# Kernel tuning notes

Measured on AMD Instinct MI355X. Metric: run time of the kernel, lower is better.

## Reference

```python
import jax, jax.numpy as jnp
import numpy as np

POOL_SIZE = 4
MAX_DIM = 256
GRID = MAX_DIM // POOL_SIZE  # 64
NUM_CELLS = GRID * GRID      # 4096
B = 64                        # static max_batch (batch.max()+1 in torch)
N = 1_000_000
C = 64


def setup_inputs() -> dict:
    key = jax.random.key(0)
    k1, k2, k3 = jax.random.split(key, 3)
    x = jax.random.normal(k1, (N, C), dtype=jnp.float32)
    pos = jax.random.randint(k2, (N, 2), 0, MAX_DIM, dtype=jnp.int64)
    batch = jnp.sort(jax.random.randint(k3, (N,), 0, B, dtype=jnp.int64))
    return {"x": x, "pos": pos, "batch": batch}


def reference(x, pos, batch):
    # voxel key: (batch, pos_x//pool, pos_y//pool) -> flat cell index
    qpos = pos[:, :2] // POOL_SIZE                       # [N, 2] int
    idx = batch * NUM_CELLS + qpos[:, 0] * GRID + qpos[:, 1]  # [N]
    num_seg = B * NUM_CELLS
    # scatter_reduce(amax, include_self=False): max over points in each cell
    pooled = jax.ops.segment_max(x, idx, num_segments=num_seg)  # empty -> -inf
    # cells with no points stay zero (output_x initialized to zeros in torch)
    counts = jax.ops.segment_sum(jnp.ones((x.shape[0], 1), x.dtype), idx,
                                 num_segments=num_seg)          # [num_seg, 1]
    pooled = jnp.where(counts > 0, pooled, jnp.zeros((), x.dtype))
    # [B, grid^2, C] -> flatten -> [B, grid^2 * C]
    return pooled.reshape(B, NUM_CELLS * x.shape[1])
```

## Files before the change

kernel.cpp:

```cpp
#include <hip/hip_runtime.h>

#define POOL_SHIFT 2
#define GRID_DIM 64
#define NUM_CELLS 4096
#define NCH 64
#define BATCH 64
#define NSEG (BATCH * NUM_CELLS)
#define SCAN_BLOCKS 1024
#define RANK_BITS 14
#define RANK_MASK ((1u << RANK_BITS) - 1u)

typedef float vf4 __attribute__((ext_vector_type(4)));

__global__ __launch_bounds__(256) void count_kernel(
    const int* __restrict__ pos, const int* __restrict__ batch,
    unsigned int* __restrict__ counts, unsigned int* __restrict__ cellrank, int n) {
    int stride = gridDim.x * blockDim.x;
    for (int p = blockIdx.x * blockDim.x + threadIdx.x; p < n; p += stride) {
        long long t = __builtin_nontemporal_load((const long long*)pos + p);
        int px = (int)t;
        int py = (int)(t >> 32);
        int b  = __builtin_nontemporal_load(&batch[p]);
        int c  = b * NUM_CELLS + (px >> POOL_SHIFT) * GRID_DIM + (py >> POOL_SHIFT);
        unsigned int r = atomicAdd(&counts[c], 1u);
        __builtin_nontemporal_store(((unsigned int)c << RANK_BITS) | r, &cellrank[p]);
    }
}

__global__ __launch_bounds__(256) void reduce_kernel(
    const unsigned int* __restrict__ counts, unsigned int* __restrict__ blocksum) {
    __shared__ unsigned int ws[4];
    int t = threadIdx.x;
    unsigned int v = counts[blockIdx.x * 256 + t];
    #pragma unroll
    for (int off = 1; off < 64; off <<= 1) v += __shfl_xor((int)v, off, 64);
    if ((t & 63) == 0) ws[t >> 6] = v;
    __syncthreads();
    if (t == 0) blocksum[blockIdx.x] = ws[0] + ws[1] + ws[2] + ws[3];
}

__global__ __launch_bounds__(1024) void scanblock_kernel(
    const unsigned int* __restrict__ blocksum, unsigned int* __restrict__ blockbase) {
    __shared__ unsigned int wsum[16];
    int t = threadIdx.x, lane = t & 63, w = t >> 6;
    unsigned int own = blocksum[t];
    unsigned int v = own;
    #pragma unroll
    for (int off = 1; off < 64; off <<= 1) {
        unsigned int u = __shfl_up((int)v, off, 64);
        if (lane >= off) v += u;
    }
    if (lane == 63) wsum[w] = v;
    __syncthreads();
    unsigned int base = 0;
    for (int i = 0; i < w; ++i) base += wsum[i];
    blockbase[t] = v + base - own;
}

__global__ __launch_bounds__(256) void offsets_kernel(
    const unsigned int* __restrict__ counts, const unsigned int* __restrict__ blockbase,
    unsigned int* __restrict__ offsets, int n) {
    __shared__ unsigned int wsum[4];
    int t = threadIdx.x, b = blockIdx.x, lane = t & 63, w = t >> 6;
    unsigned int own = counts[b * 256 + t];
    unsigned int v = own;
    #pragma unroll
    for (int off = 1; off < 64; off <<= 1) {
        unsigned int u = __shfl_up((int)v, off, 64);
        if (lane >= off) v += u;
    }
    if (lane == 63) wsum[w] = v;
    __syncthreads();
    unsigned int base = blockbase[b];
    for (int i = 0; i < w; ++i) base += wsum[i];
    unsigned int incl = v + base;
    offsets[b * 256 + t] = incl - own;
    if (b == SCAN_BLOCKS - 1 && t == 255) offsets[NSEG] = incl;
}

__global__ __launch_bounds__(256) void reorder_kernel(
    const unsigned int* __restrict__ cellrank,
    const unsigned int* __restrict__ offsets, unsigned int* __restrict__ order, int n) {
    int stride = gridDim.x * blockDim.x;
    for (int p = blockIdx.x * blockDim.x + threadIdx.x; p < n; p += stride) {
        unsigned int u = __builtin_nontemporal_load(&cellrank[p]);
        unsigned int c = u >> RANK_BITS;
        order[offsets[c] + (u & RANK_MASK)] = (unsigned int)p;
    }
}

__global__ __launch_bounds__(256) void gather_kernel(
    const float* __restrict__ x, const unsigned int* __restrict__ offsets,
    const unsigned int* __restrict__ order, float* __restrict__ out) {
    int t = threadIdx.x;
    int lane = t & 63;
    int rg = lane >> 4;
    int cg = lane & 15;
    int gw = (int)((blockIdx.x * blockDim.x + t) >> 6);
    int nw = (int)((gridDim.x * blockDim.x) >> 6);
    const float NEG_INF = -__builtin_inff();

    for (int cell = gw; cell < NSEG; cell += nw) {
        unsigned int s = offsets[cell];
        unsigned int e = offsets[cell + 1];
        size_t ob = (size_t)cell * NCH + (size_t)cg * 4;
        if (s == e) {
            if (lane < 16) {
                vf4 z = (vf4)(0.0f);
                __builtin_nontemporal_store(z, (vf4*)&out[ob]);
            }
            continue;
        }
        vf4 acc = (vf4)(NEG_INF);
        for (unsigned int base = s; base < e; base += 64) {
            unsigned int rem = e - base;
            unsigned int cnt = rem < 64u ? rem : 64u;
            unsigned int li = (unsigned int)lane < cnt ? (unsigned int)lane : cnt - 1u;
            unsigned int myp = order[base + li];

            for (unsigned int j = 0; j < cnt; j += 4) {
                unsigned int rr = j + (unsigned int)rg;
                if (rr >= cnt) rr = cnt - 1u;
                unsigned int p = (unsigned int)__shfl((int)myp, (int)rr, 64);
                vf4 v = __builtin_nontemporal_load(
                    (const vf4*)&x[(size_t)p * NCH + (size_t)cg * 4]);
                acc.x = fmaxf(acc.x, v.x);
                acc.y = fmaxf(acc.y, v.y);
                acc.z = fmaxf(acc.z, v.z);
                acc.w = fmaxf(acc.w, v.w);
            }
        }
        #pragma unroll
        for (int off = 16; off < 64; off <<= 1) {
            acc.x = fmaxf(acc.x, __shfl_xor(acc.x, off, 64));
            acc.y = fmaxf(acc.y, __shfl_xor(acc.y, off, 64));
            acc.z = fmaxf(acc.z, __shfl_xor(acc.z, off, 64));
            acc.w = fmaxf(acc.w, __shfl_xor(acc.w, off, 64));
        }
        if (lane < 16) {
            __builtin_nontemporal_store(acc, (vf4*)&out[ob]);
        }
    }
}

extern "C" void kernel_launch(void* const* d_in, const int* in_sizes, int n_in,
                              void* d_out, int out_size, void* d_ws, size_t ws_size,
                              hipStream_t stream) {
    const float* x   = (const float*)d_in[0];
    const int* pos   = (const int*)d_in[1];
    const int* batch = (const int*)d_in[2];
    float* out = (float*)d_out;
    int n = in_sizes[2];

    unsigned int* counts    = (unsigned int*)d_ws;
    unsigned int* offsets   = counts + NSEG;
    unsigned int* blocksum  = offsets + NSEG + 1;
    unsigned int* blockbase = blocksum + 1024;
    unsigned int* cellrank  = blockbase + 1024;
    unsigned int* order     = cellrank + n;

    (void)hipMemsetAsync(counts, 0, (size_t)NSEG * sizeof(unsigned int), stream);

    count_kernel<<<4096, 256, 0, stream>>>(pos, batch, counts, cellrank, n);
    reduce_kernel<<<SCAN_BLOCKS, 256, 0, stream>>>(counts, blocksum);
    scanblock_kernel<<<1, 1024, 0, stream>>>(blocksum, blockbase);
    offsets_kernel<<<SCAN_BLOCKS, 256, 0, stream>>>(counts, blockbase, offsets, n);
    reorder_kernel<<<4096, 256, 0, stream>>>(cellrank, offsets, order, n);
    gather_kernel<<<2048, 256, 0, stream>>>(x, offsets, order, out);
}
```

Before: 434.9 us.

## Fuse all pipeline stages into one cooperative kernel with grid syncs

Replaces the memset and six separate kernel launches with a single cooperative persistent kernel that zeroes counts, counts points, scans, reorders and gathers, separated by grid-wide barriers. The scan is restructured so per-chunk local scans are written directly and then fixed up with block bases. This is meant to remove launch overheads and inter-kernel gaps. In exchange it relies on grid.sync costs, caps the grid at the occupancy-limited block count, and adds a launch_bounds occupancy hint.

```diff
diff --git a/kernel.cpp b/kernel.cpp
--- a/kernel.cpp
+++ b/kernel.cpp
@@ -1,4 +1,7 @@
 #include <hip/hip_runtime.h>
+#include <hip/hip_cooperative_groups.h>
+
+namespace cg = cooperative_groups;
 
 #define POOL_SHIFT 2
 #define GRID_DIM 64
@@ -6,104 +9,102 @@
 #define NCH 64
 #define BATCH 64
 #define NSEG (BATCH * NUM_CELLS)
-#define SCAN_BLOCKS 1024
+#define CHUNKS 1024
 #define RANK_BITS 14
 #define RANK_MASK ((1u << RANK_BITS) - 1u)
 
 typedef float vf4 __attribute__((ext_vector_type(4)));
 
-__global__ __launch_bounds__(256) void count_kernel(
-    const int* __restrict__ pos, const int* __restrict__ batch,
-    unsigned int* __restrict__ counts, unsigned int* __restrict__ cellrank, int n) {
-    int stride = gridDim.x * blockDim.x;
-    for (int p = blockIdx.x * blockDim.x + threadIdx.x; p < n; p += stride) {
-        long long t = __builtin_nontemporal_load((const long long*)pos + p);
-        int px = (int)t;
-        int py = (int)(t >> 32);
+__global__ __launch_bounds__(256, 8) void fused_kernel(
+    const float* __restrict__ x, const int* __restrict__ pos,
+    const int* __restrict__ batch, float* __restrict__ out,
+    unsigned int* __restrict__ counts, unsigned int* __restrict__ offsets,
+    unsigned int* __restrict__ blocksum, unsigned int* __restrict__ blockbase,
+    unsigned int* __restrict__ cellrank, unsigned int* __restrict__ order,
+    int n)
+{
+    cg::grid_group grid = cg::this_grid();
+    const int t = threadIdx.x;
+    const int T = (int)(gridDim.x * blockDim.x);
+    const int gtid = (int)(blockIdx.x * blockDim.x + t);
+    const int lane = t & 63;
+    const int w = t >> 6;
+    __shared__ unsigned int wsum[4];
+
+    for (int i = gtid; i < NSEG; i += T) counts[i] = 0u;
+    grid.sync();
+
+    for (int p = gtid; p < n; p += T) {
+        long long pr = __builtin_nontemporal_load((const long long*)pos + p);
+        int px = (int)pr;
+        int py = (int)(pr >> 32);
         int b  = __builtin_nontemporal_load(&batch[p]);
         int c  = b * NUM_CELLS + (px >> POOL_SHIFT) * GRID_DIM + (py >> POOL_SHIFT);
         unsigned int r = atomicAdd(&counts[c], 1u);
         __builtin_nontemporal_store(((unsigned int)c << RANK_BITS) | r, &cellrank[p]);
     }
-}
+    grid.sync();
 
-__global__ __launch_bounds__(256) void reduce_kernel(
-    const unsigned int* __restrict__ counts, unsigned int* __restrict__ blocksum) {
-    __shared__ unsigned int ws[4];
-    int t = threadIdx.x;
-    unsigned int v = counts[blockIdx.x * 256 + t];
-    #pragma unroll
-    for (int off = 1; off < 64; off <<= 1) v += __shfl_xor((int)v, off, 64);
-    if ((t & 63) == 0) ws[t >> 6] = v;
-    __syncthreads();
-    if (t == 0) blocksum[blockIdx.x] = ws[0] + ws[1] + ws[2] + ws[3];
-}
+    for (int b = blockIdx.x; b < CHUNKS; b += (int)gridDim.x) {
+        unsigned int own = counts[b * 256 + t];
+        unsigned int v = own;
+        #pragma unroll
+        for (int off = 1; off < 64; off <<= 1) {
+            unsigned int u = __shfl_up((int)v, off, 64);
+            if (lane >= off) v += u;
+        }
+        if (lane == 63) wsum[w] = v;
+        __syncthreads();
+        unsigned int base = 0;
+        for (int i = 0; i < w; ++i) base += wsum[i];
+        offsets[b * 256 + t] = v + base - own;
+        if (t == 255) blocksum[b] = v + base;
+        __syncthreads();
+    }
+    grid.sync();
 
-__global__ __launch_bounds__(1024) void scanblock_kernel(
-    const unsigned int* __restrict__ blocksum, unsigned int* __restrict__ blockbase) {
-    __shared__ unsigned int wsum[16];
-    int t = threadIdx.x, lane = t & 63, w = t >> 6;
-    unsigned int own = blocksum[t];
-    unsigned int v = own;
-    #pragma unroll
-    for (int off = 1; off < 64; off <<= 1) {
-        unsigned int u = __shfl_up((int)v, off, 64);
-        if (lane >= off) v += u;
+    if (blockIdx.x == 0) {
+        unsigned int v0 = blocksum[t * 4 + 0], v1 = blocksum[t * 4 + 1];
+        unsigned int v2 = blocksum[t * 4 + 2], v3 = blocksum[t * 4 + 3];
+        unsigned int s0 = v0, s1 = s0 + v1, s2 = s1 + v2, tot = s2 + v3;
+        unsigned int v = tot;
+        #pragma unroll
+        for (int off = 1; off < 64; off <<= 1) {
+            unsigned int u = __shfl_up((int)v, off, 64);
+            if (lane >= off) v += u;
+        }
+        if (lane == 63) wsum[w] = v;
+        __syncthreads();
+        unsigned int base = 0;
+        for (int i = 0; i < w; ++i) base += wsum[i];
+        unsigned int ex = v + base - tot;
+        blockbase[t * 4 + 0] = ex;
+        blockbase[t * 4 + 1] = ex + s0;
+        blockbase[t * 4 + 2] = ex + s1;
+        blockbase[t * 4 + 3] = ex + s2;
     }
-    if (lane == 63) wsum[w] = v;
-    __syncthreads();
-    unsigned int base = 0;
-    for (int i = 0; i < w; ++i) base += wsum[i];
-    blockbase[t] = v + base - own;
-}
+    grid.sync();
 
-__global__ __launch_bounds__(256) void offsets_kernel(
-    const unsigned int* __restrict__ counts, const unsigned int* __restrict__ blockbase,
-    unsigned int* __restrict__ offsets, int n) {
-    __shared__ unsigned int wsum[4];
-    int t = threadIdx.x, b = blockIdx.x, lane = t & 63, w = t >> 6;
-    unsigned int own = counts[b * 256 + t];
-    unsigned int v = own;
-    #pragma unroll
-    for (int off = 1; off < 64; off <<= 1) {
-        unsigned int u = __shfl_up((int)v, off, 64);
-        if (lane >= off) v += u;
+    for (int i = gtid; i < NSEG; i += T) offsets[i] += blockbase[i >> 8];
+    if (gtid == 0) offsets[NSEG] = (unsigned int)n;
+    grid.sync();
+
+    for (int p = gtid; p < n; p += T) {
+        unsigned int u = __builtin_nontemporal_load(&cellrank[p]);
+        order[offsets[u >> RANK_BITS] + (u & RANK_MASK)] = (unsigned int)p;
     }
-    if (lane == 63) wsum[w] = v;
-    __syncthreads();
-    unsigned int base = blockbase[b];
-    for (int i = 0; i < w; ++i) base += wsum[i];
-    unsigned int incl = v + base;
-    offsets[b * 256 + t] = incl - own;
-    if (b == SCAN_BLOCKS - 1 && t == 255) offsets[NSEG] = incl;
-}
+    grid.sync();
 
-__global__ __launch_bounds__(256) void reorder_kernel(
-    const unsigned int* __restrict__ cellrank,
-    const unsigned int* __restrict__ offsets, unsigned int* __restrict__ order, int n) {
-    int stride = gridDim.x * blockDim.x;
-    for (int p = blockIdx.x * blockDim.x + threadIdx.x; p < n; p += stride) {
-        unsigned int u = __builtin_nontemporal_load(&cellrank[p]);
-        unsigned int c = u >> RANK_BITS;
-        order[offsets[c] + (u & RANK_MASK)] = (unsigned int)p;
-    }
-}
-
-__global__ __launch_bounds__(256) void gather_kernel(
-    const float* __restrict__ x, const unsigned int* __restrict__ offsets,
-    const unsigned int* __restrict__ order, float* __restrict__ out) {
-    int t = threadIdx.x;
-    int lane = t & 63;
-    int rg = lane >> 4;
-    int cg = lane & 15;
-    int gw = (int)((blockIdx.x * blockDim.x + t) >> 6);
-    int nw = (int)((gridDim.x * blockDim.x) >> 6);
+    const int rg = lane >> 4;
+    const int cgch = lane & 15;
+    const int gw = gtid >> 6;
+    const int nw = T >> 6;
     const float NEG_INF = -__builtin_inff();
 
     for (int cell = gw; cell < NSEG; cell += nw) {
         unsigned int s = offsets[cell];
         unsigned int e = offsets[cell + 1];
-        size_t ob = (size_t)cell * NCH + (size_t)cg * 4;
+        size_t ob = (size_t)cell * NCH + (size_t)cgch * 4;
         if (s == e) {
             if (lane < 16) {
                 vf4 z = (vf4)(0.0f);
@@ -123,7 +124,7 @@
                 if (rr >= cnt) rr = cnt - 1u;
                 unsigned int p = (unsigned int)__shfl((int)myp, (int)rr, 64);
                 vf4 v = __builtin_nontemporal_load(
-                    (const vf4*)&x[(size_t)p * NCH + (size_t)cg * 4]);
+                    (const vf4*)&x[(size_t)p * NCH + (size_t)cgch * 4]);
                 acc.x = fmaxf(acc.x, v.x);
                 acc.y = fmaxf(acc.y, v.y);
                 acc.z = fmaxf(acc.z, v.z);
@@ -159,12 +160,18 @@
     unsigned int* cellrank  = blockbase + 1024;
     unsigned int* order     = cellrank + n;
 
-    (void)hipMemsetAsync(counts, 0, (size_t)NSEG * sizeof(unsigned int), stream);
+    static int g_blocks = 0;
+    if (g_blocks == 0) {
+        int nb = 0;
+        (void)hipOccupancyMaxActiveBlocksPerMultiprocessor(&nb, fused_kernel, 256, 0);
+        if (nb < 1) nb = 1;
+        g_blocks = nb * 256;
+        if (g_blocks > 2048) g_blocks = 2048;
+    }
 
-    count_kernel<<<4096, 256, 0, stream>>>(pos, batch, counts, cellrank, n);
-    reduce_kernel<<<SCAN_BLOCKS, 256, 0, stream>>>(counts, blocksum);
-    scanblock_kernel<<<1, 1024, 0, stream>>>(blocksum, blockbase);
-    offsets_kernel<<<SCAN_BLOCKS, 256, 0, stream>>>(counts, blockbase, offsets, n);
-    reorder_kernel<<<4096, 256, 0, stream>>>(cellrank, offsets, order, n);
-    gather_kernel<<<2048, 256, 0, stream>>>(x, offsets, order, out);
+    void* args[] = {(void*)&x, (void*)&pos, (void*)&batch, (void*)&out,
+                    (void*)&counts, (void*)&offsets, (void*)&blocksum,
+                    (void*)&blockbase, (void*)&cellrank, (void*)&order, (void*)&n};
+    (void)hipLaunchCooperativeKernel((const void*)fused_kernel, dim3(g_blocks),
+                                     dim3(256), args, 0, stream);
 }
```

Measured after the change: 1.575 ms. 3.62x slower.

## Assign four cells per wavefront in gather, one 16-lane group per cell

Applied to the files above, without the earlier changes.

The gather kernel now maps each 16-lane subgroup of a wavefront to its own cell, so a wave handles four cells at once instead of splitting one cell's points across four row groups. This drops the cross-group shuffle reduction and the per-chunk order load and shuffle broadcast. Each subgroup walks its cell's point list directly, unrolled by four to keep several row loads in flight. The trade-off is divergence when cells in the same wave hold very different point counts, and the nontemporal hint on loads of x is removed.

```diff
diff --git a/kernel.cpp b/kernel.cpp
--- a/kernel.cpp
+++ b/kernel.cpp
@@ -94,52 +94,45 @@
     const unsigned int* __restrict__ order, float* __restrict__ out) {
     int t = threadIdx.x;
     int lane = t & 63;
-    int rg = lane >> 4;
-    int cg = lane & 15;
+    int sub = lane >> 4;
+    int cg  = lane & 15;
     int gw = (int)((blockIdx.x * blockDim.x + t) >> 6);
     int nw = (int)((gridDim.x * blockDim.x) >> 6);
     const float NEG_INF = -__builtin_inff();
 
-    for (int cell = gw; cell < NSEG; cell += nw) {
-        unsigned int s = offsets[cell];
-        unsigned int e = offsets[cell + 1];
-        size_t ob = (size_t)cell * NCH + (size_t)cg * 4;
-        if (s == e) {
-            if (lane < 16) {
-                vf4 z = (vf4)(0.0f);
-                __builtin_nontemporal_store(z, (vf4*)&out[ob]);
-            }
-            continue;
+    for (int g = gw; g < NSEG / 4; g += nw) {
+        int c = g * 4 + sub;
+        unsigned int s = offsets[c];
+        unsigned int e = offsets[c + 1];
+        unsigned int cnt = e - s;
+        vf4 acc = (vf4)(NEG_INF);
+
+        unsigned int k = 0;
+        for (; k + 4 <= cnt; k += 4) {
+            unsigned int p0 = order[s + k];
+            unsigned int p1 = order[s + k + 1];
+            unsigned int p2 = order[s + k + 2];
+            unsigned int p3 = order[s + k + 3];
+            vf4 v0 = *(const vf4*)&x[(size_t)p0 * NCH + (size_t)cg * 4];
+            vf4 v1 = *(const vf4*)&x[(size_t)p1 * NCH + (size_t)cg * 4];
+            vf4 v2 = *(const vf4*)&x[(size_t)p2 * NCH + (size_t)cg * 4];
+            vf4 v3 = *(const vf4*)&x[(size_t)p3 * NCH + (size_t)cg * 4];
+            acc.x = fmaxf(fmaxf(fmaxf(acc.x, v0.x), fmaxf(v1.x, v2.x)), v3.x);
+            acc.y = fmaxf(fmaxf(fmaxf(acc.y, v0.y), fmaxf(v1.y, v2.y)), v3.y);
+            acc.z = fmaxf(fmaxf(fmaxf(acc.z, v0.z), fmaxf(v1.z, v2.z)), v3.z);
+            acc.w = fmaxf(fmaxf(fmaxf(acc.w, v0.w), fmaxf(v1.w, v2.w)), v3.w);
         }
-        vf4 acc = (vf4)(NEG_INF);
-        for (unsigned int base = s; base < e; base += 64) {
-            unsigned int rem = e - base;
-            unsigned int cnt = rem < 64u ? rem : 64u;
-            unsigned int li = (unsigned int)lane < cnt ? (unsigned int)lane : cnt - 1u;
-            unsigned int myp = order[base + li];
-
-            for (unsigned int j = 0; j < cnt; j += 4) {
-                unsigned int rr = j + (unsigned int)rg;
-                if (rr >= cnt) rr = cnt - 1u;
-                unsigned int p = (unsigned int)__shfl((int)myp, (int)rr, 64);
-                vf4 v = __builtin_nontemporal_load(
-                    (const vf4*)&x[(size_t)p * NCH + (size_t)cg * 4]);
-                acc.x = fmaxf(acc.x, v.x);
-                acc.y = fmaxf(acc.y, v.y);
-                acc.z = fmaxf(acc.z, v.z);
-                acc.w = fmaxf(acc.w, v.w);
-            }
+        for (; k < cnt; ++k) {
+            unsigned int p = order[s + k];
+            vf4 v = *(const vf4*)&x[(size_t)p * NCH + (size_t)cg * 4];
+            acc.x = fmaxf(acc.x, v.x);
+            acc.y = fmaxf(acc.y, v.y);
+            acc.z = fmaxf(acc.z, v.z);
+            acc.w = fmaxf(acc.w, v.w);
         }
-        #pragma unroll
-        for (int off = 16; off < 64; off <<= 1) {
-            acc.x = fmaxf(acc.x, __shfl_xor(acc.x, off, 64));
-            acc.y = fmaxf(acc.y, __shfl_xor(acc.y, off, 64));
-            acc.z = fmaxf(acc.z, __shfl_xor(acc.z, off, 64));
-            acc.w = fmaxf(acc.w, __shfl_xor(acc.w, off, 64));
-        }
-        if (lane < 16) {
-            __builtin_nontemporal_store(acc, (vf4*)&out[ob]);
-        }
+        if (cnt == 0u) acc = (vf4)(0.0f);
+        __builtin_nontemporal_store(
+            acc, (vf4*)&out[(size_t)c * NCH + (size_t)cg * 4]);
     }
 }
 
```

Result: no change. 433.9 us (-0.2%).
